# Kernel tuning notes

Hardware: AMD Instinct MI355X
Metric: run time of the kernel (lower is better)

## Reference

```python
import jax, jax.numpy as jnp
import numpy as np

V, E, U = 50257, 256, 256
B, T = 32, 512


def setup_inputs() -> dict:
    key = jax.random.key(0)
    ks = jax.random.split(key, 8)
    s = 0.02  # small init keeps relu-LSTM numerically stable over 512 steps
    return {
        "tokens": jax.random.randint(ks[0], (B, T), 0, V, dtype=jnp.int32),
        "emb": jax.random.normal(ks[1], (V, E), jnp.float32) * s,
        "Wk_f": jax.random.normal(ks[2], (E, 4 * U), jnp.float32) * s,
        "Wr_f": jax.random.normal(ks[3], (U, 4 * U), jnp.float32) * s,
        "b_f": jnp.zeros((4 * U,), jnp.float32),
        "Wk_b": jax.random.normal(ks[4], (E, 4 * U), jnp.float32) * s,
        "Wr_b": jax.random.normal(ks[5], (U, 4 * U), jnp.float32) * s,
        "b_b": jnp.zeros((4 * U,), jnp.float32),
    }


def _lstm_relu(xw, mask, Wr):
    """xw: [T,B,4U] precomputed x@Wk+b; mask: [T,B,1] bool; Wr: [U,4U].
    Keras LSTM with activation='relu', recurrent_activation='sigmoid',
    gate order i,f,g,o. Masked steps carry state & output."""
    u = Wr.shape[0]
    b = xw.shape[1]
    h0 = jnp.zeros((b, u), xw.dtype)
    c0 = jnp.zeros((b, u), xw.dtype)

    def step(carry, inp):
        h, c = carry
        z_x, m = inp
        z = z_x + h @ Wr  # [B,4U]
        i, f, g, o = jnp.split(z, 4, axis=-1)
        i = jax.nn.sigmoid(i)
        f = jax.nn.sigmoid(f)
        g = jax.nn.relu(g)
        o = jax.nn.sigmoid(o)
        c_new = f * c + i * g
        h_new = o * jax.nn.relu(c_new)
        h2 = jnp.where(m, h_new, h)
        c2 = jnp.where(m, c_new, c)
        return (h2, c2), h2

    (hT, cT), ys = jax.lax.scan(step, (h0, c0), (xw, mask))
    return ys, hT, cT  # ys: [T,B,U]


def reference(tokens, emb, Wk_f, Wr_f, b_f, Wk_b, Wr_b, b_b):
    x = emb[tokens]                    # [B,T,E]
    mask = (tokens != 0)[..., None]    # [B,T,1] mask_zero=True
    # forward direction
    xw_f = (x @ Wk_f + b_f).transpose(1, 0, 2)   # [T,B,4U]
    m_f = mask.transpose(1, 0, 2)                # [T,B,1]
    ys_f, hf, cf = _lstm_relu(xw_f, m_f, Wr_f)
    # backward direction: reversed sequence, then re-reverse outputs
    xw_b = (x @ Wk_b + b_b)[:, ::-1].transpose(1, 0, 2)
    m_b = mask[:, ::-1].transpose(1, 0, 2)
    ys_b, hb, cb = _lstm_relu(xw_b, m_b, Wr_b)
    ys_b = ys_b[::-1]
    encoder_outputs = jnp.concatenate([ys_f, ys_b], axis=-1).transpose(1, 0, 2)  # [B,T,2U]
    # NOTE: original module concatenates f_state_h with b_state_c (bug kept faithfully)
    encoder_state_h = jnp.concatenate([hf, cb], axis=-1)  # [B,2U]
    encoder_state_c = jnp.concatenate([cf, cb], axis=-1)  # [B,2U]
    return encoder_outputs, encoder_state_h, encoder_state_c
```

## Files before the change

kernel.cpp:

```cpp
#include <hip/hip_runtime.h>
#include <hip/hip_bf16.h>

#define TT 512
#define BB 32
#define EE 256
#define UU 256
#define NG 1024

typedef unsigned int u32;
typedef unsigned long long u64;
typedef unsigned short u16;
typedef __attribute__((ext_vector_type(8))) short short8;
typedef __attribute__((ext_vector_type(4))) float f32x4;

#define TAGMASK 0x0000FFFF0000FFFFull

__device__ __forceinline__ float bf2f(u16 u) { return __uint_as_float(((u32)u) << 16); }
__device__ __forceinline__ u16 f2bf(float f) {
    u32 x = __float_as_uint(f);
    u32 r = (x + 0x7fffu + ((x >> 16) & 1u)) >> 16;
    return (u16)r;
}

__launch_bounds__(256)
__global__ void xw_gemm(const int* __restrict__ tokens,
                        const float* __restrict__ emb,
                        const float* __restrict__ Wk_f, const float* __restrict__ b_f,
                        const float* __restrict__ Wk_b, const float* __restrict__ b_b,
                        u16* __restrict__ xw)
{
    const int dir = blockIdx.z;
    const float* Wk   = dir ? Wk_b : Wk_f;
    const float* bias = dir ? b_b  : b_f;
    const int bn = blockIdx.x;
    const int bm = blockIdx.y;
    const int tid = threadIdx.x;

    __shared__ __align__(16) float At[32][68];
    __shared__ __align__(16) float Bs[32][132];

    float acc[8][4];
#pragma unroll
    for (int i = 0; i < 8; i++)
#pragma unroll
        for (int j = 0; j < 4; j++) acc[i][j] = 0.f;

    const int tx = tid & 31;
    const int ty = tid >> 5;
    const int c0 = tx * 4;
    const int r0 = ty * 8;

    const int lr = tid >> 3;
    const int lk = (tid & 7) * 4;

    for (int k0 = 0; k0 < EE; k0 += 32) {
#pragma unroll
        for (int p = 0; p < 2; p++) {
            int r = lr + p * 32;
            int row = bm * 64 + r;
            int tok = tokens[row];
            const float4 v = *reinterpret_cast<const float4*>(&emb[(size_t)tok * EE + k0 + lk]);
            At[lk + 0][r] = v.x; At[lk + 1][r] = v.y; At[lk + 2][r] = v.z; At[lk + 3][r] = v.w;
        }
        {
            int ck = (tid & 31) * 4;
            int kk = tid >> 5;
#pragma unroll
            for (int p = 0; p < 4; p++) {
                int k = kk + p * 8;
                const float4 v = *reinterpret_cast<const float4*>(&Wk[(size_t)(k0 + k) * NG + bn * 128 + ck]);
                *reinterpret_cast<float4*>(&Bs[k][ck]) = v;
            }
        }
        __syncthreads();
#pragma unroll 8
        for (int k = 0; k < 32; k++) {
            float4 a0 = *reinterpret_cast<const float4*>(&At[k][r0]);
            float4 a1 = *reinterpret_cast<const float4*>(&At[k][r0 + 4]);
            float4 b0 = *reinterpret_cast<const float4*>(&Bs[k][c0]);
            float a[8] = {a0.x, a0.y, a0.z, a0.w, a1.x, a1.y, a1.z, a1.w};
            float b[4] = {b0.x, b0.y, b0.z, b0.w};
#pragma unroll
            for (int i = 0; i < 8; i++)
#pragma unroll
                for (int j = 0; j < 4; j++)
                    acc[i][j] = fmaf(a[i], b[j], acc[i][j]);
        }
        __syncthreads();
    }

    float4 bv = *reinterpret_cast<const float4*>(&bias[bn * 128 + c0]);
    float bias4[4] = {bv.x, bv.y, bv.z, bv.w};
    const int cbase = bn * 128 + c0;
    const int gate  = cbase >> 8;
    const int unitv = cbase & 255;
    const int ugx   = unitv >> 5;
    const int wcol  = gate * 32 + (unitv & 31);
#pragma unroll
    for (int i = 0; i < 8; i++) {
        int row = bm * 64 + r0 + i;
        int b = row >> 9;
        int t = row & 511;
        int t2 = dir ? (TT - 1 - t) : t;
        size_t base = ((((size_t)(dir * TT + t2)) * 8 + ugx) * BB + b) * 128 + wcol;
        ushort4 st;
        st.x = f2bf(acc[i][0] + bias4[0]);
        st.y = f2bf(acc[i][1] + bias4[1]);
        st.z = f2bf(acc[i][2] + bias4[2]);
        st.w = f2bf(acc[i][3] + bias4[3]);
        *reinterpret_cast<ushort4*>(&xw[base]) = st;
    }
}

__device__ __forceinline__ u64 ld_agent(const u64* p) {
    return __hip_atomic_load(p, __ATOMIC_RELAXED, __HIP_MEMORY_SCOPE_AGENT);
}

__launch_bounds__(256, 1)
__global__ void lstm_rec(const int* __restrict__ tokens,
                         const u16* __restrict__ xw,
                         const float* __restrict__ Wr_f,
                         const float* __restrict__ Wr_b,
                         u64* __restrict__ hgq,
                         float* __restrict__ out)
{
    const int wg  = blockIdx.x;
    const int dir = wg >> 3;
    const int ug  = wg & 7;
    const int unit0 = ug * 32;
    const int tid = threadIdx.x;
    const int wv  = tid >> 6;
    const int l   = tid & 63;

    __shared__ __align__(16) u32   HsW[32 * 128];
    __shared__ __align__(16) float Zs[2][BB][132];

    const float* Wr = dir ? Wr_b : Wr_f;
    short8 bfrag[8][2];
    {
        const int col = wv * UU + unit0 + (l & 15);
#pragma unroll
        for (int kt = 0; kt < 8; kt++) {
#pragma unroll
            for (int nt = 0; nt < 2; nt++) {
                int k0 = kt * 32 + (l >> 4) * 8;
                short8 v;
#pragma unroll
                for (int jj = 0; jj < 8; jj++)
                    v[jj] = (short)f2bf(Wr[(size_t)(k0 + jj) * NG + col + nt * 16]);
                bfrag[kt][nt] = v;
            }
        }
    }

    const int cb = tid >> 3;
    const int cj = tid & 7;
    float c_st[4] = {0.f, 0.f, 0.f, 0.f};
    float h_st[4] = {0.f, 0.f, 0.f, 0.f};

    const u16* xwD = xw + (size_t)dir * TT * 8 * BB * 128;
    u64 pxw[4];
    int ptok;
    {
        const u16* p = xwD + (((size_t)0 * 8 + ug) * BB + cb) * 128 + cj * 4;
#pragma unroll
        for (int g = 0; g < 4; g++)
            pxw[g] = *reinterpret_cast<const u64*>(p + g * 32);
        ptok = tokens[cb * TT + (dir ? (TT - 1) : 0)];
    }

    float* outs_h = out + (size_t)BB * TT * 512;
    float* outs_c = outs_h + (size_t)BB * 512;

    u64 qa[16];

    for (int s = 0; s < TT; s++) {
        const int p = s & 1;
        f32x4 acc[2][2];
#pragma unroll
        for (int mt = 0; mt < 2; mt++)
#pragma unroll
            for (int nt = 0; nt < 2; nt++) acc[mt][nt] = (f32x4){0.f, 0.f, 0.f, 0.f};

        if (s > 0) {
            const u64* hb = hgq + (size_t)(p * 2 + dir) * 4096 + wv * 1024 + l;
            const u64 tp = (u64)(u32)s | ((u64)(u32)s << 32);
            int rounds = 0;
            for (;;) {
                u64 qb[16];
#pragma unroll
                for (int j = 0; j < 16; j++) qb[j] = ld_agent(hb + j * 64);
                __builtin_amdgcn_sched_barrier(0);
                u64 bad = 0;
#pragma unroll
                for (int j = 0; j < 16; j++) bad |= qa[j] ^ tp;
                if (__all((bad & TAGMASK) == 0ull)) break;
#pragma unroll
                for (int j = 0; j < 16; j++) qa[j] = qb[j];
                if (++rounds > 4) __builtin_amdgcn_s_sleep(1);
            }
#pragma unroll
            for (int j = 0; j < 16; j++) {
                u32 w32 = (((u32)(qa[j] >> 16)) & 0xFFFFu) | (((u32)(qa[j] >> 48)) << 16);
                int ugs = wv * 2 + (j >> 3);
                int b   = (j * 4 + (l >> 4)) & 31;
                int pos = l & 15;
                int g   = ugs * 4 + (pos >> 2);
                HsW[b * 128 + ((g ^ (b & 7)) << 2) + (pos & 3)] = w32;
            }
            __syncthreads();

#pragma unroll
            for (int kt = 0; kt < 8; kt++) {
#pragma unroll
                for (int mt = 0; mt < 2; mt++) {
                    int b = mt * 16 + (l & 15);
                    int g = kt * 4 + (l >> 4);
                    short8 af = *reinterpret_cast<const short8*>(
                        &HsW[b * 128 + ((g ^ (b & 7)) << 2)]);
                    acc[mt][0] = __builtin_amdgcn_mfma_f32_16x16x32_bf16(af, bfrag[kt][0], acc[mt][0], 0, 0, 0);
                    acc[mt][1] = __builtin_amdgcn_mfma_f32_16x16x32_bf16(af, bfrag[kt][1], acc[mt][1], 0, 0, 0);
                }
            }
        }

#pragma unroll
        for (int mt = 0; mt < 2; mt++)
#pragma unroll
            for (int nt = 0; nt < 2; nt++)
#pragma unroll
                for (int r = 0; r < 4; r++)
                    Zs[p][mt * 16 + (l >> 4) * 4 + r][wv * 32 + nt * 16 + (l & 15)] = acc[mt][nt][r];
        __syncthreads();

        float h2[4], c2[4];
        {
            const bool m = (ptok != 0);
#pragma unroll
            for (int q = 0; q < 4; q++) {
                float zi = Zs[p][cb][0 * 32 + cj * 4 + q] + bf2f((u16)(pxw[0] >> (16 * q)));
                float zf = Zs[p][cb][1 * 32 + cj * 4 + q] + bf2f((u16)(pxw[1] >> (16 * q)));
                float zg = Zs[p][cb][2 * 32 + cj * 4 + q] + bf2f((u16)(pxw[2] >> (16 * q)));
                float zo = Zs[p][cb][3 * 32 + cj * 4 + q] + bf2f((u16)(pxw[3] >> (16 * q)));
                float ii = 1.f / (1.f + __expf(-zi));
                float ff = 1.f / (1.f + __expf(-zf));
                float gg = fmaxf(zg, 0.f);
                float oo = 1.f / (1.f + __expf(-zo));
                float cn = ff * c_st[q] + ii * gg;
                float hn = oo * fmaxf(cn, 0.f);
                h2[q] = m ? hn : h_st[q];
                c2[q] = m ? cn : c_st[q];
                h_st[q] = h2[q];
                c_st[q] = c2[q];
            }
        }

        {
            const u32 tagn = (u32)(s + 1);
            u32 t0 = ((u32)f2bf(h2[0]) << 16) | tagn;
            u32 t1 = ((u32)f2bf(h2[1]) << 16) | tagn;
            u32 t2 = ((u32)f2bf(h2[2]) << 16) | tagn;
            u32 t3 = ((u32)f2bf(h2[3]) << 16) | tagn;
            u64 lo = (u64)t0 | ((u64)t1 << 32);
            u64 hi = (u64)t2 | ((u64)t3 << 32);
            u64* hd = hgq + (size_t)(((s + 1) & 1) * 2 + dir) * 4096 + (ug * 32 + cb) * 16 + cj * 2;
            __hip_atomic_store(hd + 0, lo, __ATOMIC_RELAXED, __HIP_MEMORY_SCOPE_AGENT);
            __hip_atomic_store(hd + 1, hi, __ATOMIC_RELAXED, __HIP_MEMORY_SCOPE_AGENT);
        }

        if (s + 1 < TT) {
            const u64* hb2 = hgq + (size_t)((((s + 1) & 1)) * 2 + dir) * 4096 + wv * 1024 + l;
#pragma unroll
            for (int j = 0; j < 16; j++) qa[j] = ld_agent(hb2 + j * 64);
            __builtin_amdgcn_sched_barrier(0);
        }

        const int tv = dir ? (TT - 1 - s) : s;
        *reinterpret_cast<float4*>(&out[((size_t)cb * TT + tv) * 512 + dir * UU + unit0 + cj * 4]) =
            make_float4(h2[0], h2[1], h2[2], h2[3]);
        if (s == TT - 1) {
            if (dir == 0) {
                *reinterpret_cast<float4*>(&outs_h[cb * 512 + unit0 + cj * 4]) = make_float4(h2[0], h2[1], h2[2], h2[3]);
                *reinterpret_cast<float4*>(&outs_c[cb * 512 + unit0 + cj * 4]) = make_float4(c2[0], c2[1], c2[2], c2[3]);
            } else {
                *reinterpret_cast<float4*>(&outs_h[cb * 512 + UU + unit0 + cj * 4]) = make_float4(c2[0], c2[1], c2[2], c2[3]);
                *reinterpret_cast<float4*>(&outs_c[cb * 512 + UU + unit0 + cj * 4]) = make_float4(c2[0], c2[1], c2[2], c2[3]);
            }
        }
        if (s + 1 < TT) {
            const u16* px = xwD + (((size_t)(s + 1) * 8 + ug) * BB + cb) * 128 + cj * 4;
#pragma unroll
            for (int g = 0; g < 4; g++)
                pxw[g] = *reinterpret_cast<const u64*>(px + g * 32);
            ptok = tokens[cb * TT + (dir ? (TT - 2 - s) : (s + 1))];
        }
    }
}

extern "C" void kernel_launch(void* const* d_in, const int* in_sizes, int n_in,
                              void* d_out, int out_size, void* d_ws, size_t ws_size,
                              hipStream_t stream) {
    const int*   tokens = (const int*)d_in[0];
    const float* emb    = (const float*)d_in[1];
    const float* Wk_f   = (const float*)d_in[2];
    const float* Wr_f   = (const float*)d_in[3];
    const float* b_f    = (const float*)d_in[4];
    const float* Wk_b   = (const float*)d_in[5];
    const float* Wr_b   = (const float*)d_in[6];
    const float* b_b    = (const float*)d_in[7];
    float* out = (float*)d_out;

    char* ws = (char*)d_ws;
    u16* xw  = (u16*)ws;
    u64* hgq = (u64*)(ws + 67108864);

    (void)hipMemsetAsync(hgq, 0, 131072, stream);
    dim3 g1(8, 256, 2);
    xw_gemm<<<g1, 256, 0, stream>>>(tokens, emb, Wk_f, b_f, Wk_b, b_b, xw);
    lstm_rec<<<16, 256, 0, stream>>>(tokens, xw, Wr_f, Wr_b, hgq, out);
}
```

Measured before the change: 2.085 ms.

## Restructure LSTM recurrence to 4 WGs per direction with all-gate MFMA tiles

The recurrent kernel now uses 4 workgroups per direction instead of 8. Each wave computes all four gates for 16 units directly in MFMA accumulators, so the Zs shared-memory round trip and one barrier per step go away. Each workgroup writes its own h slice to local LDS and starts the MFMAs on its local K chunk before polling the global flags for the other workgroups' slices, overlapping the cross-workgroup wait with compute. In exchange there are fewer CUs doing the per-step matmul and more MFMA work per wave, and correctness depends on the new polling layout and double-buffered LDS.

```diff
diff --git a/kernel.cpp b/kernel.cpp
--- a/kernel.cpp
+++ b/kernel.cpp
@@ -12,6 +12,7 @@
 typedef unsigned short u16;
 typedef __attribute__((ext_vector_type(8))) short short8;
 typedef __attribute__((ext_vector_type(4))) float f32x4;
+typedef __attribute__((ext_vector_type(4))) u32 u32x4;
 
 #define TAGMASK 0x0000FFFF0000FFFFull
 
@@ -124,175 +125,227 @@
                          u64* __restrict__ hgq,
                          float* __restrict__ out)
 {
-    const int wg  = blockIdx.x;
-    const int dir = wg >> 3;
-    const int ug  = wg & 7;
-    const int unit0 = ug * 32;
+    const int wq  = blockIdx.x;
+    const int dir = wq >> 2;
+    const int w   = wq & 3;
     const int tid = threadIdx.x;
     const int wv  = tid >> 6;
     const int l   = tid & 63;
 
-    __shared__ __align__(16) u32   HsW[32 * 128];
-    __shared__ __align__(16) float Zs[2][BB][132];
+    __shared__ __align__(16) u32 HsW[2][32 * 128];
 
     const float* Wr = dir ? Wr_b : Wr_f;
-    short8 bfrag[8][2];
+
+    short8 wfrag[8][4];
     {
-        const int col = wv * UU + unit0 + (l & 15);
-#pragma unroll
-        for (int kt = 0; kt < 8; kt++) {
-#pragma unroll
-            for (int nt = 0; nt < 2; nt++) {
+        const int col = w * 64 + wv * 16 + (l & 15);
+#pragma unroll
+        for (int kt = 0; kt < 8; kt++)
+#pragma unroll
+            for (int g = 0; g < 4; g++) {
                 int k0 = kt * 32 + (l >> 4) * 8;
                 short8 v;
 #pragma unroll
-                for (int jj = 0; jj < 8; jj++)
-                    v[jj] = (short)f2bf(Wr[(size_t)(k0 + jj) * NG + col + nt * 16]);
-                bfrag[kt][nt] = v;
-            }
-        }
-    }
-
-    const int cb = tid >> 3;
-    const int cj = tid & 7;
-    float c_st[4] = {0.f, 0.f, 0.f, 0.f};
-    float h_st[4] = {0.f, 0.f, 0.f, 0.f};
+                for (int j = 0; j < 8; j++)
+                    v[j] = (short)f2bf(Wr[(size_t)(k0 + j) * NG + g * 256 + col]);
+                wfrag[kt][g] = v;
+            }
+    }
+
+    const int ubase = w * 64 + wv * 16 + ((l >> 4) << 2);
+    const int bl    = l & 15;
+    const int ug    = ubase >> 5;
+    const int uo    = ubase & 31;
+    const int lp0   = ubase >> 1;
+    const int gl    = lp0 >> 2;
+    const int slotb = lp0 & 3;
+    const int bq = tid & 31;
+    const int gq = tid >> 5;
+    int gg3[3];
+#pragma unroll
+    for (int i = 0; i < 3; i++) { int gi = i * 8 + gq; gg3[i] = (gi < w * 8) ? gi : gi + 8; }
+
+    float h_st[2][4], c_st[2][4];
+#pragma unroll
+    for (int nb = 0; nb < 2; nb++)
+#pragma unroll
+        for (int r = 0; r < 4; r++) { h_st[nb][r] = 0.f; c_st[nb][r] = 0.f; }
 
     const u16* xwD = xw + (size_t)dir * TT * 8 * BB * 128;
-    u64 pxw[4];
-    int ptok;
-    {
-        const u16* p = xwD + (((size_t)0 * 8 + ug) * BB + cb) * 128 + cj * 4;
-#pragma unroll
-        for (int g = 0; g < 4; g++)
-            pxw[g] = *reinterpret_cast<const u64*>(p + g * 32);
-        ptok = tokens[cb * TT + (dir ? (TT - 1) : 0)];
+    u64 pxw[4][2];
+    int ptok[2];
+#pragma unroll
+    for (int nb = 0; nb < 2; nb++) {
+        int b = nb * 16 + bl;
+        const u16* p = xwD + (((size_t)0 * 8 + ug) * BB + b) * 128 + uo;
+#pragma unroll
+        for (int g = 0; g < 4; g++) pxw[g][nb] = *reinterpret_cast<const u64*>(p + g * 32);
+        ptok[nb] = tokens[b * TT + (dir ? (TT - 1) : 0)];
     }
 
     float* outs_h = out + (size_t)BB * TT * 512;
     float* outs_c = outs_h + (size_t)BB * 512;
 
-    u64 qa[16];
+    u64 qp[12];
 
     for (int s = 0; s < TT; s++) {
-        const int p = s & 1;
-        f32x4 acc[2][2];
-#pragma unroll
-        for (int mt = 0; mt < 2; mt++)
-#pragma unroll
-            for (int nt = 0; nt < 2; nt++) acc[mt][nt] = (f32x4){0.f, 0.f, 0.f, 0.f};
+        f32x4 acc[4][2];
+#pragma unroll
+        for (int g = 0; g < 4; g++)
+#pragma unroll
+            for (int nb = 0; nb < 2; nb++) acc[g][nb] = (f32x4){0.f, 0.f, 0.f, 0.f};
 
         if (s > 0) {
-            const u64* hb = hgq + (size_t)(p * 2 + dir) * 4096 + wv * 1024 + l;
-            const u64 tp = (u64)(u32)s | ((u64)(u32)s << 32);
-            int rounds = 0;
-            for (;;) {
-                u64 qb[16];
-#pragma unroll
-                for (int j = 0; j < 16; j++) qb[j] = ld_agent(hb + j * 64);
-                __builtin_amdgcn_sched_barrier(0);
-                u64 bad = 0;
-#pragma unroll
-                for (int j = 0; j < 16; j++) bad |= qa[j] ^ tp;
-                if (__all((bad & TAGMASK) == 0ull)) break;
-#pragma unroll
-                for (int j = 0; j < 16; j++) qa[j] = qb[j];
-                if (++rounds > 4) __builtin_amdgcn_s_sleep(1);
-            }
-#pragma unroll
-            for (int j = 0; j < 16; j++) {
-                u32 w32 = (((u32)(qa[j] >> 16)) & 0xFFFFu) | (((u32)(qa[j] >> 48)) << 16);
-                int ugs = wv * 2 + (j >> 3);
-                int b   = (j * 4 + (l >> 4)) & 31;
-                int pos = l & 15;
-                int g   = ugs * 4 + (pos >> 2);
-                HsW[b * 128 + ((g ^ (b & 7)) << 2) + (pos & 3)] = w32;
-            }
-            __syncthreads();
-
-#pragma unroll
-            for (int kt = 0; kt < 8; kt++) {
-#pragma unroll
-                for (int mt = 0; mt < 2; mt++) {
-                    int b = mt * 16 + (l & 15);
-                    int g = kt * 4 + (l >> 4);
+            u32* Hb = HsW[s & 1];
+#pragma unroll
+            for (int kk = 0; kk < 2; kk++) {
+                int kt = w * 2 + kk;
+#pragma unroll
+                for (int nb = 0; nb < 2; nb++) {
+                    int b = nb * 16 + bl;
+                    int gk = kt * 4 + (l >> 4);
                     short8 af = *reinterpret_cast<const short8*>(
-                        &HsW[b * 128 + ((g ^ (b & 7)) << 2)]);
-                    acc[mt][0] = __builtin_amdgcn_mfma_f32_16x16x32_bf16(af, bfrag[kt][0], acc[mt][0], 0, 0, 0);
-                    acc[mt][1] = __builtin_amdgcn_mfma_f32_16x16x32_bf16(af, bfrag[kt][1], acc[mt][1], 0, 0, 0);
-                }
-            }
-        }
-
-#pragma unroll
-        for (int mt = 0; mt < 2; mt++)
-#pragma unroll
-            for (int nt = 0; nt < 2; nt++)
-#pragma unroll
-                for (int r = 0; r < 4; r++)
-                    Zs[p][mt * 16 + (l >> 4) * 4 + r][wv * 32 + nt * 16 + (l & 15)] = acc[mt][nt][r];
-        __syncthreads();
-
-        float h2[4], c2[4];
-        {
-            const bool m = (ptok != 0);
-#pragma unroll
-            for (int q = 0; q < 4; q++) {
-                float zi = Zs[p][cb][0 * 32 + cj * 4 + q] + bf2f((u16)(pxw[0] >> (16 * q)));
-                float zf = Zs[p][cb][1 * 32 + cj * 4 + q] + bf2f((u16)(pxw[1] >> (16 * q)));
-                float zg = Zs[p][cb][2 * 32 + cj * 4 + q] + bf2f((u16)(pxw[2] >> (16 * q)));
-                float zo = Zs[p][cb][3 * 32 + cj * 4 + q] + bf2f((u16)(pxw[3] >> (16 * q)));
+                        &Hb[b * 128 + ((gk ^ (b & 7)) << 2)]);
+#pragma unroll
+                    for (int g = 0; g < 4; g++)
+                        acc[g][nb] = __builtin_amdgcn_mfma_f32_16x16x32_bf16(wfrag[kt][g], af, acc[g][nb], 0, 0, 0);
+                }
+            }
+            {
+                const u64 tp = (u64)(u32)s | ((u64)(u32)s << 32);
+                const u64* pol = hgq + ((size_t)((s & 1) * 2 + dir) * 32 + bq) * 128;
+                int rounds = 0;
+                for (;;) {
+                    u64 bad = 0;
+#pragma unroll
+                    for (int i = 0; i < 12; i++) bad |= qp[i] ^ tp;
+                    if (__all((bad & TAGMASK) == 0ull)) break;
+                    if (++rounds > 2) __builtin_amdgcn_s_sleep(1);
+#pragma unroll
+                    for (int i = 0; i < 3; i++)
+#pragma unroll
+                        for (int j = 0; j < 4; j++)
+                            qp[i * 4 + j] = ld_agent(pol + gg3[i] * 4 + j);
+                }
+#pragma unroll
+                for (int i = 0; i < 3; i++) {
+                    u32x4 v4;
+#pragma unroll
+                    for (int j = 0; j < 4; j++) {
+                        u64 q = qp[i * 4 + j];
+                        v4[j] = (u32)((q >> 16) & 0xFFFFu) | ((u32)(q >> 48) << 16);
+                    }
+                    *reinterpret_cast<u32x4*>(&Hb[bq * 128 + ((gg3[i] ^ (bq & 7)) << 2)]) = v4;
+                }
+            }
+            asm volatile("s_waitcnt lgkmcnt(0)" ::: "memory");
+            __builtin_amdgcn_s_barrier();
+#pragma unroll
+            for (int kk = 0; kk < 6; kk++) {
+                int kt = (kk < w * 2) ? kk : kk + 2;
+#pragma unroll
+                for (int nb = 0; nb < 2; nb++) {
+                    int b = nb * 16 + bl;
+                    int gk = kt * 4 + (l >> 4);
+                    short8 af = *reinterpret_cast<const short8*>(
+                        &Hb[b * 128 + ((gk ^ (b & 7)) << 2)]);
+#pragma unroll
+                    for (int g = 0; g < 4; g++)
+                        acc[g][nb] = __builtin_amdgcn_mfma_f32_16x16x32_bf16(wfrag[kt][g], af, acc[g][nb], 0, 0, 0);
+                }
+            }
+        }
+
+        float h2[2][4], c2[2][4];
+#pragma unroll
+        for (int nb = 0; nb < 2; nb++) {
+            const bool m = (ptok[nb] != 0);
+#pragma unroll
+            for (int r = 0; r < 4; r++) {
+                float zi = acc[0][nb][r] + bf2f((u16)(pxw[0][nb] >> (16 * r)));
+                float zf = acc[1][nb][r] + bf2f((u16)(pxw[1][nb] >> (16 * r)));
+                float zg = acc[2][nb][r] + bf2f((u16)(pxw[2][nb] >> (16 * r)));
+                float zo = acc[3][nb][r] + bf2f((u16)(pxw[3][nb] >> (16 * r)));
                 float ii = 1.f / (1.f + __expf(-zi));
                 float ff = 1.f / (1.f + __expf(-zf));
                 float gg = fmaxf(zg, 0.f);
                 float oo = 1.f / (1.f + __expf(-zo));
-                float cn = ff * c_st[q] + ii * gg;
+                float cn = ff * c_st[nb][r] + ii * gg;
                 float hn = oo * fmaxf(cn, 0.f);
-                h2[q] = m ? hn : h_st[q];
-                c2[q] = m ? cn : c_st[q];
-                h_st[q] = h2[q];
-                c_st[q] = c2[q];
-            }
-        }
-
-        {
+                h2[nb][r] = m ? hn : h_st[nb][r];
+                c2[nb][r] = m ? cn : c_st[nb][r];
+                h_st[nb][r] = h2[nb][r];
+                c_st[nb][r] = c2[nb][r];
+            }
+        }
+
+        if (s + 1 < TT) {
             const u32 tagn = (u32)(s + 1);
-            u32 t0 = ((u32)f2bf(h2[0]) << 16) | tagn;
-            u32 t1 = ((u32)f2bf(h2[1]) << 16) | tagn;
-            u32 t2 = ((u32)f2bf(h2[2]) << 16) | tagn;
-            u32 t3 = ((u32)f2bf(h2[3]) << 16) | tagn;
-            u64 lo = (u64)t0 | ((u64)t1 << 32);
-            u64 hi = (u64)t2 | ((u64)t3 << 32);
-            u64* hd = hgq + (size_t)(((s + 1) & 1) * 2 + dir) * 4096 + (ug * 32 + cb) * 16 + cj * 2;
-            __hip_atomic_store(hd + 0, lo, __ATOMIC_RELAXED, __HIP_MEMORY_SCOPE_AGENT);
-            __hip_atomic_store(hd + 1, hi, __ATOMIC_RELAXED, __HIP_MEMORY_SCOPE_AGENT);
-        }
-
+            u64* st = hgq + ((size_t)(((s + 1) & 1) * 2 + dir) * 32) * 128;
+#pragma unroll
+            for (int nb = 0; nb < 2; nb++) {
+                int b = nb * 16 + bl;
+#pragma unroll
+                for (int pr = 0; pr < 2; pr++) {
+                    u32 qlo = ((u32)f2bf(h2[nb][2 * pr + 0]) << 16) | tagn;
+                    u32 qhi = ((u32)f2bf(h2[nb][2 * pr + 1]) << 16) | tagn;
+                    __hip_atomic_store(st + (size_t)b * 128 + lp0 + pr,
+                                       (u64)qlo | ((u64)qhi << 32),
+                                       __ATOMIC_RELAXED, __HIP_MEMORY_SCOPE_AGENT);
+                }
+            }
+            u32* Hn = HsW[(s + 1) & 1];
+#pragma unroll
+            for (int nb = 0; nb < 2; nb++) {
+                int b = nb * 16 + bl;
+                u32 w0 = (u32)f2bf(h2[nb][0]) | ((u32)f2bf(h2[nb][1]) << 16);
+                u32 w1 = (u32)f2bf(h2[nb][2]) | ((u32)f2bf(h2[nb][3]) << 16);
+                *reinterpret_cast<u64*>(&Hn[b * 128 + ((gl ^ (b & 7)) << 2) + slotb]) =
+                    (u64)w0 | ((u64)w1 << 32);
+            }
+            const u64* pol2 = hgq + ((size_t)(((s + 1) & 1) * 2 + dir) * 32 + bq) * 128;
+#pragma unroll
+            for (int i = 0; i < 3; i++)
+#pragma unroll
+                for (int j = 0; j < 4; j++)
+                    qp[i * 4 + j] = ld_agent(pol2 + gg3[i] * 4 + j);
+        }
+
+        const int tv = dir ? (TT - 1 - s) : s;
+#pragma unroll
+        for (int nb = 0; nb < 2; nb++) {
+            int b = nb * 16 + bl;
+            *reinterpret_cast<f32x4*>(&out[((size_t)b * TT + tv) * 512 + dir * UU + ubase]) =
+                (f32x4){h2[nb][0], h2[nb][1], h2[nb][2], h2[nb][3]};
+        }
+        if (s == TT - 1) {
+#pragma unroll
+            for (int nb = 0; nb < 2; nb++) {
+                int b = nb * 16 + bl;
+                if (dir == 0) {
+                    *reinterpret_cast<f32x4*>(&outs_h[b * 512 + ubase]) =
+                        (f32x4){h2[nb][0], h2[nb][1], h2[nb][2], h2[nb][3]};
+                    *reinterpret_cast<f32x4*>(&outs_c[b * 512 + ubase]) =
+                        (f32x4){c2[nb][0], c2[nb][1], c2[nb][2], c2[nb][3]};
+                } else {
+                    *reinterpret_cast<f32x4*>(&outs_h[b * 512 + UU + ubase]) =
+                        (f32x4){c2[nb][0], c2[nb][1], c2[nb][2], c2[nb][3]};
+                    *reinterpret_cast<f32x4*>(&outs_c[b * 512 + UU + ubase]) =
+                        (f32x4){c2[nb][0], c2[nb][1], c2[nb][2], c2[nb][3]};
+                }
+            }
+        }
         if (s + 1 < TT) {
-            const u64* hb2 = hgq + (size_t)((((s + 1) & 1)) * 2 + dir) * 4096 + wv * 1024 + l;
-#pragma unroll
-            for (int j = 0; j < 16; j++) qa[j] = ld_agent(hb2 + j * 64);
-            __builtin_amdgcn_sched_barrier(0);
-        }
-
-        const int tv = dir ? (TT - 1 - s) : s;
-        *reinterpret_cast<float4*>(&out[((size_t)cb * TT + tv) * 512 + dir * UU + unit0 + cj * 4]) =
-            make_float4(h2[0], h2[1], h2[2], h2[3]);
-        if (s == TT - 1) {
-            if (dir == 0) {
-                *reinterpret_cast<float4*>(&outs_h[cb * 512 + unit0 + cj * 4]) = make_float4(h2[0], h2[1], h2[2], h2[3]);
-                *reinterpret_cast<float4*>(&outs_c[cb * 512 + unit0 + cj * 4]) = make_float4(c2[0], c2[1], c2[2], c2[3]);
-            } else {
-                *reinterpret_cast<float4*>(&outs_h[cb * 512 + UU + unit0 + cj * 4]) = make_float4(c2[0], c2[1], c2[2], c2[3]);
-                *reinterpret_cast<float4*>(&outs_c[cb * 512 + UU + unit0 + cj * 4]) = make_float4(c2[0], c2[1], c2[2], c2[3]);
-            }
-        }
-        if (s + 1 < TT) {
-            const u16* px = xwD + (((size_t)(s + 1) * 8 + ug) * BB + cb) * 128 + cj * 4;
-#pragma unroll
-            for (int g = 0; g < 4; g++)
-                pxw[g] = *reinterpret_cast<const u64*>(px + g * 32);
-            ptok = tokens[cb * TT + (dir ? (TT - 2 - s) : (s + 1))];
+#pragma unroll
+            for (int nb = 0; nb < 2; nb++) {
+                int b = nb * 16 + bl;
+                const u16* p = xwD + (((size_t)(s + 1) * 8 + ug) * BB + b) * 128 + uo;
+#pragma unroll
+                for (int g = 0; g < 4; g++) pxw[g][nb] = *reinterpret_cast<const u64*>(p + g * 32);
+                ptok[nb] = tokens[b * TT + (dir ? (TT - 2 - s) : (s + 1))];
+            }
+            asm volatile("s_waitcnt lgkmcnt(0)" ::: "memory");
+            __builtin_amdgcn_s_barrier();
         }
     }
 }
@@ -317,5 +370,5 @@
     (void)hipMemsetAsync(hgq, 0, 131072, stream);
     dim3 g1(8, 256, 2);
     xw_gemm<<<g1, 256, 0, stream>>>(tokens, emb, Wk_f, b_f, Wk_b, b_b, xw);
-    lstm_rec<<<16, 256, 0, stream>>>(tokens, xw, Wr_f, Wr_b, hgq, out);
-}
+    lstm_rec<<<8, 256, 0, stream>>>(tokens, xw, Wr_f, Wr_b, hgq, out);
+}
```

Result: slower. 5.723 ms (+174.5%).
